# Optimization experiments

Hardware: AMD Instinct MI355X
Metric: run time of the kernel (lower is better)

## Reference

```python
import jax, jax.numpy as jnp
import numpy as np

D = 1024   # input_size == hidden_size (tied weights)
H = 1024
V = 32000
STEPS = 5  # mogrify_steps
B = 32
T = 64


def _mogrify(x, h, W, b):
    # W: [STEPS, H, H] (square since D == H), b: [STEPS, H]
    for i in range(STEPS):
        if (i + 1) % 2 == 0:
            h = 2.0 * jax.nn.sigmoid(x @ W[i].T + b[i]) * h
        else:
            x = 2.0 * jax.nn.sigmoid(h @ W[i].T + b[i]) * x
    return x, h


def _lstm_cell(x, h, c, W_ih, W_hh, b_ih, b_hh):
    g = x @ W_ih.T + b_ih + h @ W_hh.T + b_hh  # [B, 4H], gate order i,f,g,o
    i, f, gg, o = jnp.split(g, 4, axis=-1)
    c = jax.nn.sigmoid(f) * c + jax.nn.sigmoid(i) * jnp.tanh(gg)
    h = jax.nn.sigmoid(o) * jnp.tanh(c)
    return h, c


def setup_inputs() -> dict:
    key = jax.random.key(0)
    ks = jax.random.split(key, 16)
    s = 1.0 / np.sqrt(H)
    u = lambda k, shape: jax.random.uniform(k, shape, jnp.float32, -s, s)
    return {
        "seq": jax.random.randint(ks[0], (B, T), 0, V),
        "max_len": T,
        "emb": jax.random.normal(ks[1], (V, D), jnp.float32) * 0.02,  # tied with fc weight
        "mog1_W": u(ks[2], (STEPS, H, H)), "mog1_b": u(ks[3], (STEPS, H)),
        "W_ih1": u(ks[4], (4 * H, D)), "W_hh1": u(ks[5], (4 * H, H)),
        "b_ih1": u(ks[6], (4 * H,)), "b_hh1": u(ks[7], (4 * H,)),
        "mog2_W": u(ks[8], (STEPS, H, H)), "mog2_b": u(ks[9], (STEPS, H)),
        "W_ih2": u(ks[10], (4 * H, H)), "W_hh2": u(ks[11], (4 * H, H)),
        "b_ih2": u(ks[12], (4 * H,)), "b_hh2": u(ks[13], (4 * H,)),
        "fc_b": u(ks[14], (V,)),
    }


def reference(seq, max_len, emb, mog1_W, mog1_b, W_ih1, W_hh1, b_ih1, b_hh1,
              mog2_W, mog2_b, W_ih2, W_hh2, b_ih2, b_hh2, fc_b):
    batch = seq.shape[0]
    embed = emb[seq[:, :max_len]]              # [B, T, D]
    xs = jnp.transpose(embed, (1, 0, 2))       # [T, B, D]
    h1 = jnp.zeros((batch, H), embed.dtype)
    c1 = jnp.zeros((batch, H), embed.dtype)
    h2 = jnp.zeros((batch, H), embed.dtype)
    c2 = jnp.zeros((batch, H), embed.dtype)

    def step(carry, x):
        h1, c1, h2, c2 = carry
        x1, h1m = _mogrify(x, h1, mog1_W, mog1_b)
        h1, c1 = _lstm_cell(x1, h1m, c1, W_ih1, W_hh1, b_ih1, b_hh1)
        x2, h2m = _mogrify(h1, h2, mog2_W, mog2_b)
        h2, c2 = _lstm_cell(x2, h2m, c2, W_ih2, W_hh2, b_ih2, b_hh2)
        return (h1, c1, h2, c2), h2

    _, hs = jax.lax.scan(step, (h1, c1, h2, c2), xs)   # hs: [T, B, H]
    hidden_states = jnp.transpose(hs, (1, 0, 2))        # [B, T, H]
    # fc weight tied to embedding -> logits = h @ emb.T + b (single big GEMM)
    outputs = jnp.einsum('bth,vh->btv', hidden_states, emb) + fc_b  # [B, T, V]
    return outputs, hidden_states
```

## Files before the change

### kernel.cpp

```cpp
#include <hip/hip_runtime.h>

typedef short bf16x8 __attribute__((ext_vector_type(8)));
typedef float f32x4 __attribute__((ext_vector_type(4)));
typedef unsigned int u32;
typedef u32 u32x4 __attribute__((ext_vector_type(4)));
typedef unsigned short u16;
typedef unsigned long long u64;

static __device__ __forceinline__ unsigned short f2bf(float f) {
    unsigned int u = __float_as_uint(f);
    unsigned int r = (u + 0x7fffu + ((u >> 16) & 1u)) >> 16;
    return (unsigned short)r;
}
static __device__ __forceinline__ float sigmoidf_(float x) {
    return 1.0f / (1.0f + __expf(-x));
}
static __device__ __forceinline__ float tanhf_(float x) {
    return 2.0f / (1.0f + __expf(-2.0f * x)) - 1.0f;
}

static __device__ __forceinline__ u32 pkhi(float a, float b) {
    return (__float_as_uint(a) >> 16) | (__float_as_uint(b) & 0xffff0000u);
}
static __device__ __forceinline__ u32 pklo(float a, float b) {
    float la = a - __uint_as_float(__float_as_uint(a) & 0xffff0000u);
    float lb = b - __uint_as_float(__float_as_uint(b) & 0xffff0000u);
    return (__float_as_uint(la) >> 16) | (__float_as_uint(lb) & 0xffff0000u);
}
static __device__ __forceinline__ bf16x8 mkfrag(u32 a, u32 b, u32 c, u32 d) {
    u32x4 v = {a, b, c, d};
    return __builtin_bit_cast(bf16x8, v);
}

static __device__ __forceinline__ bf16x8 ldA(const u16* p) {
    u64 a = __hip_atomic_load((const u64*)p, __ATOMIC_RELAXED, __HIP_MEMORY_SCOPE_AGENT);
    u64 b = __hip_atomic_load((const u64*)(p + 4), __ATOMIC_RELAXED, __HIP_MEMORY_SCOPE_AGENT);
    union { u64 q[2]; bf16x8 v; } u;
    u.q[0] = a; u.q[1] = b;
    return u.v;
}
static __device__ __forceinline__ float ldc4(const float* p) {
    return __hip_atomic_load(p, __ATOMIC_RELAXED, __HIP_MEMORY_SCOPE_AGENT);
}
static __device__ __forceinline__ void stc4(float* p, float v) {
    __hip_atomic_store(p, v, __ATOMIC_RELAXED, __HIP_MEMORY_SCOPE_AGENT);
}
static __device__ __forceinline__ void stc2(u16* p, u16 v) {
    __hip_atomic_store(p, v, __ATOMIC_RELAXED, __HIP_MEMORY_SCOPE_AGENT);
}

static __device__ __forceinline__ void dma16(const float* g, float* l) {
    __builtin_amdgcn_global_load_lds((const __attribute__((address_space(1))) void*)g,
                                     (__attribute__((address_space(3))) void*)l, 16, 0, 0);
}

static __device__ __forceinline__ void arrD(u32* bar, int line) {
    asm volatile("s_waitcnt vmcnt(0) lgkmcnt(0)" ::: "memory");
    __builtin_amdgcn_s_barrier();
    if (threadIdx.x == 0)
        __hip_atomic_fetch_add(bar + line * 32, 1u, __ATOMIC_RELAXED, __HIP_MEMORY_SCOPE_AGENT);
}
static __device__ __forceinline__ void arrP(u32* bar, int line) {
    __builtin_amdgcn_s_barrier();
    if (threadIdx.x == 0)
        __hip_atomic_fetch_add(bar + line * 32, 1u, __ATOMIC_RELAXED, __HIP_MEMORY_SCOPE_AGENT);
}
static __device__ __forceinline__ void bwaitSD(u32* bar, int layer, bool glob, u32 target) {
    if (threadIdx.x < 64) {
        const bool on = glob || (threadIdx.x < 32);
        const int line = glob ? (int)threadIdx.x : layer * 32 + (int)(threadIdx.x & 31);
        const u32 tgt = glob ? (target << 8) : (target << 7);
        for (;;) {
            u32 v = on ? __hip_atomic_load(bar + line * 32, __ATOMIC_RELAXED,
                                           __HIP_MEMORY_SCOPE_AGENT) : 0u;
            v += __shfl_xor(v, 1);
            v += __shfl_xor(v, 2);
            v += __shfl_xor(v, 4);
            v += __shfl_xor(v, 8);
            v += __shfl_xor(v, 16);
            v += __shfl_xor(v, 32);
            if (v >= tgt) break;
            __builtin_amdgcn_s_sleep(1);
        }
    }
    __builtin_amdgcn_s_barrier();
    asm volatile("" ::: "memory");
}

static __device__ __forceinline__ void stage_mogF(const float* W, int jb, float* lbuf,
                                                  int lane, int wv) {
    int oct2 = lane >> 5, row = (lane >> 1) & 15, half = lane & 1;
#pragma unroll
    for (int i = 0; i < 16; ++i) {
        int og = wv * 16 + i;
        const float* src = W + (size_t)(jb + row) * 1024 + (og * 2 + oct2) * 8 + half * 4;
        dma16(src, lbuf + og * 256);
    }
}
static __device__ __forceinline__ void stage_l128(const float* Ws, int jb, int kb,
                                                  float* lbuf, int lane, int wv) {
    int half = lane & 1;
#pragma unroll
    for (int i = 0; i < 8; ++i) {
        int octl = wv * 4 + (i >> 1);
        int rh = i & 1;
        int rowc = rh * 32 + (lane >> 1);
        int grow = (rowc >> 4) * 1024 + jb + (rowc & 15);
        const float* src = Ws + (size_t)grow * 1024 + kb + octl * 8 + half * 4;
        dma16(src, lbuf + octl * 512 + rh * 256);
    }
}

static __device__ __forceinline__ void l_acts(const u16* aH, const u16* aL, int cidx,
                                              int lane, int wv, bf16x8 fr[4]) {
    const int col = lane & 15, kq4 = lane >> 4;
    size_t octa = (size_t)cidx * 16 + wv * 4 + kq4;
    const u16* pH = aH + (octa * 32 + col) * 8;
    const u16* pL = aL + (octa * 32 + col) * 8;
    fr[0] = ldA(pH);
    fr[1] = ldA(pH + 128);
    fr[2] = ldA(pL);
    fr[3] = ldA(pL + 128);
}
static __device__ __forceinline__ void l_mfma(const float* lbuf, const bf16x8 fr[4],
                                              int lane, int wv, f32x4 (&acc)[4][2]) {
    const int col = lane & 15, kq4 = lane >> 4;
    const float* wbase = lbuf + (wv * 4 + kq4) * 512;
#pragma unroll
    for (int rt = 0; rt < 4; ++rt) {
        const float* wp = wbase + (rt * 16 + col) * 8;
        f32x4 w0 = *(const f32x4*)wp, w1 = *(const f32x4*)(wp + 4);
        bf16x8 whi = mkfrag(pkhi(w0.x, w0.y), pkhi(w0.z, w0.w),
                            pkhi(w1.x, w1.y), pkhi(w1.z, w1.w));
        bf16x8 wlo = mkfrag(pklo(w0.x, w0.y), pklo(w0.z, w0.w),
                            pklo(w1.x, w1.y), pklo(w1.z, w1.w));
        acc[rt][0] = __builtin_amdgcn_mfma_f32_16x16x32_bf16(fr[0], whi, acc[rt][0], 0, 0, 0);
        acc[rt][0] = __builtin_amdgcn_mfma_f32_16x16x32_bf16(fr[2], whi, acc[rt][0], 0, 0, 0);
        acc[rt][0] = __builtin_amdgcn_mfma_f32_16x16x32_bf16(fr[0], wlo, acc[rt][0], 0, 0, 0);
        acc[rt][1] = __builtin_amdgcn_mfma_f32_16x16x32_bf16(fr[1], whi, acc[rt][1], 0, 0, 0);
        acc[rt][1] = __builtin_amdgcn_mfma_f32_16x16x32_bf16(fr[3], whi, acc[rt][1], 0, 0, 0);
        acc[rt][1] = __builtin_amdgcn_mfma_f32_16x16x32_bf16(fr[1], wlo, acc[rt][1], 0, 0, 0);
    }
}

struct RArgs {
    const float *m1W, *m1b, *Wih1, *Whh1, *bih1, *bhh1;
    const float *m2W, *m2b, *Wih2, *Whh2, *bih2, *bhh2;
    float* XTF;
    u16 *XTH, *XTL;
    float* stF;
    u16* stH;
    float* hs;
    u32* bar;
};

__global__ __launch_bounds__(256, 1) void reck(RArgs A) {
    __shared__ float wbuf[4][8192];
    __shared__ float red[4][32][16];

    const int tid = threadIdx.x, lane = tid & 63, wv = tid >> 6;
    const int col = lane & 15, kq4 = lane >> 4;
    const int blk = blockIdx.x;
    const int layer = blk >> 7;
    const int g = blk & 127;
    const bool isMog = g < 64;
    const int line = layer * 32 + (g & 31);
    const int jb = (g & 63) * 16;

    const float* mW  = layer ? A.m2W : A.m1W;
    const float* mb_ = layer ? A.m2b : A.m1b;
    const float* Wih = layer ? A.Wih2 : A.Wih1;
    const float* Whh = layer ? A.Whh2 : A.Whh1;
    const float* bih = layer ? A.bih2 : A.bih1;
    const float* bhh = layer ? A.bhh2 : A.bhh1;

    float* hF  = A.stF + layer * 32768;
    float* hmF = A.stF + 65536 + layer * 32768;
    float* cS  = A.stF + 131072 + layer * 32768;
    float* rFb = A.stF + 196608;
    u16* hH  = A.stH + layer * 32768;
    u16* hmH = A.stH + 65536 + layer * 32768;
    u16* rHb = A.stH + 131072;
    u16* hL  = A.stH + 196608 + layer * 32768;
    u16* hmL = A.stH + 262144 + layer * 32768;
    u16* rLb = A.stH + 327680;

    float* mbuf0 = &wbuf[0][0];
    float* mbuf1 = &wbuf[2][0];

    u32 bcnt = 0;
    int cur = 0;

    if (isMog) stage_mogF(mW, jb, mbuf0, lane, wv);

    for (int s = 0; s <= 64; ++s) {
        const bool act = layer ? (s > 0) : (s < 64);
        const int t = layer ? s - 1 : s;
        const int tt = act ? t : 0;
        const int rb = tt & 1;

        float* xF; u16 *xH, *xL;
        if (layer == 0) {
            xF = A.XTF + (size_t)tt * 32768;
            xH = A.XTH + (size_t)tt * 32768;
            xL = A.XTL + (size_t)tt * 32768;
        } else {
            xF = rFb + rb * 32768;
            xH = rHb + rb * 32768;
            xL = rLb + rb * 32768;
        }

        if (isMog) {
            for (int ph = 0; ph < 5; ++ph) {
                float* wsrc = cur ? mbuf1 : mbuf0;
                float* wdst = cur ? mbuf0 : mbuf1;
                if (act) {
                    const u16 *gH, *gL; const float* srcF; float* dF; u16 *dH, *dL;
                    switch (ph) {
                        case 0:  gH = hH;  gL = hL;  srcF = xF;  dF = xF;  dH = xH;  dL = xL;  break;
                        case 1:  gH = xH;  gL = xL;  srcF = hF;  dF = hmF; dH = hmH; dL = hmL; break;
                        case 2:  gH = hmH; gL = hmL; srcF = xF;  dF = xF;  dH = xH;  dL = xL;  break;
                        case 3:  gH = xH;  gL = xL;  srcF = hmF; dF = hmF; dH = hmH; dL = hmL; break;
                        default: gH = hmH; gL = hmL; srcF = xF;  dF = xF;  dH = xH;  dL = xL;  break;
                    }
                    bf16x8 AH0[8], AH1[8], AL0[8], AL1[8];
#pragma unroll
                    for (int kt = 0; kt < 8; ++kt) {
                        int octc = wv * 32 + kt * 4 + kq4;
                        const u16* pH = gH + ((size_t)octc * 32 + col) * 8;
                        const u16* pL = gL + ((size_t)octc * 32 + col) * 8;
                        AH0[kt] = ldA(pH);  AH1[kt] = ldA(pH + 128);
                        AL0[kt] = ldA(pL);  AL1[kt] = ldA(pL + 128);
                    }
                    asm volatile("s_waitcnt vmcnt(63)" ::: "memory");
                    f32x4 a0 = {0.f, 0.f, 0.f, 0.f}, a1 = {0.f, 0.f, 0.f, 0.f};
#pragma unroll
                    for (int kt = 0; kt < 8; ++kt) {
                        int octc = wv * 32 + kt * 4 + kq4;
                        const float* wp = wsrc + octc * 128 + col * 8;
                        f32x4 w0 = *(const f32x4*)wp, w1 = *(const f32x4*)(wp + 4);
                        bf16x8 whi = mkfrag(pkhi(w0.x, w0.y), pkhi(w0.z, w0.w),
                                            pkhi(w1.x, w1.y), pkhi(w1.z, w1.w));
                        bf16x8 wlo = mkfrag(pklo(w0.x, w0.y), pklo(w0.z, w0.w),
                                            pklo(w1.x, w1.y), pklo(w1.z, w1.w));
                        a0 = __builtin_amdgcn_mfma_f32_16x16x32_bf16(AH0[kt], whi, a0, 0, 0, 0);
                        a0 = __builtin_amdgcn_mfma_f32_16x16x32_bf16(AL0[kt], whi, a0, 0, 0, 0);
                        a0 = __builtin_amdgcn_mfma_f32_16x16x32_bf16(AH0[kt], wlo, a0, 0, 0, 0);
                        a1 = __builtin_amdgcn_mfma_f32_16x16x32_bf16(AH1[kt], whi, a1, 0, 0, 0);
                        a1 = __builtin_amdgcn_mfma_f32_16x16x32_bf16(AL1[kt], whi, a1, 0, 0, 0);
                        a1 = __builtin_amdgcn_mfma_f32_16x16x32_bf16(AH1[kt], wlo, a1, 0, 0, 0);
                    }
#pragma unroll
                    for (int mh = 0; mh < 2; ++mh) {
                        f32x4 av = mh ? a1 : a0;
#pragma unroll
                        for (int r = 0; r < 4; ++r)
                            red[wv][mh * 16 + kq4 * 4 + r][col] = av[r];
                    }
                    __syncthreads();
#pragma unroll
                    for (int uu = 0; uu < 2; ++uu) {
                        int u = tid + uu * 256;
                        int jj = u & 15, bb = u >> 4;
                        float sv = red[0][bb][jj] + red[1][bb][jj]
                                 + red[2][bb][jj] + red[3][bb][jj];
                        int d = jb + jj;
                        sv += mb_[ph * 1024 + d];
                        float gate = 2.0f * sigmoidf_(sv);
                        size_t pidx = ((size_t)(d >> 3) * 32 + bb) * 8 + (d & 7);
                        float val = gate * ldc4(srcF + pidx);
                        stc4(dF + pidx, val);
                        u32 uv = __float_as_uint(val);
                        stc2(dH + pidx, (u16)(uv >> 16));
                        float lov = val - __uint_as_float(uv & 0xffff0000u);
                        stc2(dL + pidx, (u16)(__float_as_uint(lov) >> 16));
                    }
                    arrD(A.bar, line);
                } else {
                    arrP(A.bar, line);
                }
                ++bcnt;
                stage_mogF(mW + (size_t)((ph + 1) % 5) * 1048576, jb, wdst, lane, wv);
                bwaitSD(A.bar, layer, false, bcnt);
                cur ^= 1;
            }
            arrP(A.bar, line);
            ++bcnt;
            bwaitSD(A.bar, layer, true, bcnt);
        } else {
            const bool firstAct = act && (layer ? (s == 1) : (s == 0));
            const bool nextAct = layer ? (s < 64) : (s < 63);
            if (firstAct) {
#pragma unroll
                for (int c = 0; c < 3; ++c)
                    stage_l128(Whh, jb, c * 128, &wbuf[c][0], lane, wv);
            }
#pragma unroll
            for (int p = 0; p < 4; ++p) {
                arrP(A.bar, line);
                ++bcnt;
                bwaitSD(A.bar, layer, false, bcnt);
            }
            arrP(A.bar, line);
            ++bcnt;
            u32 g5t = bcnt;
            f32x4 acc[4][2];
#pragma unroll
            for (int rt = 0; rt < 4; ++rt) {
                acc[rt][0] = (f32x4){0.f, 0.f, 0.f, 0.f};
                acc[rt][1] = (f32x4){0.f, 0.f, 0.f, 0.f};
            }
            bf16x8 frA[4], frB[4];
            if (act) {
                l_acts(hmH, hmL, 0, lane, wv, frA);
#pragma unroll
                for (int c = 0; c < 8; ++c) {
                    if (c < 7) {
                        if (c & 1) l_acts(hmH, hmL, c + 1, lane, wv, frA);
                        else       l_acts(hmH, hmL, c + 1, lane, wv, frB);
                    }
                    asm volatile("s_waitcnt vmcnt(32)" ::: "memory");
                    int cn = c + 3;
                    if (cn < 8) stage_l128(Whh, jb, cn * 128, &wbuf[cn & 3][0], lane, wv);
                    else        stage_l128(Wih, jb, (cn - 8) * 128, &wbuf[cn & 3][0], lane, wv);
                    if (c & 1) l_mfma(&wbuf[c & 3][0], frB, lane, wv, acc);
                    else       l_mfma(&wbuf[c & 3][0], frA, lane, wv, acc);
                }
            }
            bwaitSD(A.bar, layer, false, g5t);
            if (act) {
                l_acts(xH, xL, 0, lane, wv, frA);
#pragma unroll
                for (int c = 0; c < 8; ++c) {
                    if (c < 7) {
                        if (c & 1) l_acts(xH, xL, c + 1, lane, wv, frA);
                        else       l_acts(xH, xL, c + 1, lane, wv, frB);
                    }
                    asm volatile("s_waitcnt vmcnt(32)" ::: "memory");
                    int cn = c + 3;
                    if (cn < 8) stage_l128(Wih, jb, cn * 128, &wbuf[cn & 3][0], lane, wv);
                    if (c & 1) l_mfma(&wbuf[c & 3][0], frB, lane, wv, acc);
                    else       l_mfma(&wbuf[c & 3][0], frA, lane, wv, acc);
                }
                float gv[2][4];
#pragma unroll
                for (int gt = 0; gt < 4; ++gt) {
                    __syncthreads();
#pragma unroll
                    for (int mh = 0; mh < 2; ++mh) {
                        f32x4 av = acc[gt][mh];
#pragma unroll
                        for (int r = 0; r < 4; ++r)
                            red[wv][mh * 16 + kq4 * 4 + r][col] = av[r];
                    }
                    __syncthreads();
#pragma unroll
                    for (int uu = 0; uu < 2; ++uu) {
                        int u = tid + uu * 256;
                        gv[uu][gt] = red[0][u >> 4][u & 15] + red[1][u >> 4][u & 15]
                                   + red[2][u >> 4][u & 15] + red[3][u >> 4][u & 15];
                    }
                }
#pragma unroll
                for (int uu = 0; uu < 2; ++uu) {
                    int u = tid + uu * 256;
                    int cell = u & 15, bb = u >> 4;
                    int d = jb + cell;
                    float gi = gv[uu][0] + bih[d] + bhh[d];
                    float gf = gv[uu][1] + bih[1024 + d] + bhh[1024 + d];
                    float gg = gv[uu][2] + bih[2048 + d] + bhh[2048 + d];
                    float go = gv[uu][3] + bih[3072 + d] + bhh[3072 + d];
                    int cidx = d * 32 + bb;
                    float cn = sigmoidf_(gf) * cS[cidx] + sigmoidf_(gi) * tanhf_(gg);
                    cS[cidx] = cn;
                    float hn = sigmoidf_(go) * tanhf_(cn);
                    size_t pidx = ((size_t)(d >> 3) * 32 + bb) * 8 + (d & 7);
                    u32 uv = __float_as_uint(hn);
                    u16 hhi = (u16)(uv >> 16);
                    float lov = hn - __uint_as_float(uv & 0xffff0000u);
                    u16 hlo = (u16)(__float_as_uint(lov) >> 16);
                    stc4(hF + pidx, hn);
                    stc2(hH + pidx, hhi);
                    stc2(hL + pidx, hlo);
                    if (layer == 0) {
                        int wb = s & 1;
                        stc4(rFb + wb * 32768 + pidx, hn);
                        stc2(rHb + wb * 32768 + pidx, hhi);
                        stc2(rLb + wb * 32768 + pidx, hlo);
                    } else {
                        A.hs[(size_t)bb * 65536 + (size_t)t * 1024 + d] = hn;
                    }
                }
                arrD(A.bar, line);
                ++bcnt;
                if (nextAct) {
#pragma unroll
                    for (int c = 0; c < 3; ++c)
                        stage_l128(Whh, jb, c * 128, &wbuf[c][0], lane, wv);
                }
            } else {
                arrP(A.bar, line);
                ++bcnt;
            }
            bwaitSD(A.bar, layer, true, bcnt);
        }
    }
}

__global__ __launch_bounds__(256) void gather_embed(const int* __restrict__ seq,
                                                    const float* __restrict__ emb,
                                                    float* __restrict__ XTF,
                                                    u16* __restrict__ XTH,
                                                    u16* __restrict__ XTL) {
    int t = blockIdx.x;
#pragma unroll 4
    for (int i = 0; i < 16; ++i) {
        int u = i * 256 + threadIdx.x;
        int oct = u >> 5, b = u & 31;
        int row = seq[b * 64 + t];
        const float* sp = emb + (size_t)row * 1024 + oct * 8;
        float4 f0 = *(const float4*)sp;
        float4 f1 = *(const float4*)(sp + 4);
        size_t base = (size_t)t * 32768 + ((size_t)oct * 32 + b) * 8;
        *(float4*)(XTF + base) = f0;
        *(float4*)(XTF + base + 4) = f1;
        u32x4 hi = {pkhi(f0.x, f0.y), pkhi(f0.z, f0.w), pkhi(f1.x, f1.y), pkhi(f1.z, f1.w)};
        u32x4 lo = {pklo(f0.x, f0.y), pklo(f0.z, f0.w), pklo(f1.x, f1.y), pklo(f1.z, f1.w)};
        *(u32x4*)(XTH + base) = hi;
        *(u32x4*)(XTL + base) = lo;
    }
}

__global__ __launch_bounds__(256) void f32_to_bf16(const float* __restrict__ in,
                                                   unsigned short* __restrict__ out, int n) {
    int i = (blockIdx.x * 256 + threadIdx.x) * 8;
    if (i + 7 < n) {
        float4 f0 = *(const float4*)(in + i);
        float4 f1 = *(const float4*)(in + i + 4);
        bf16x8 v;
        v[0] = (short)f2bf(f0.x); v[1] = (short)f2bf(f0.y);
        v[2] = (short)f2bf(f0.z); v[3] = (short)f2bf(f0.w);
        v[4] = (short)f2bf(f1.x); v[5] = (short)f2bf(f1.y);
        v[6] = (short)f2bf(f1.z); v[7] = (short)f2bf(f1.w);
        *(bf16x8*)(out + i) = v;
    }
}

__global__ __launch_bounds__(256) void out_proj(const unsigned short* __restrict__ hsb,
                                                const float* __restrict__ emb,
                                                const float* __restrict__ fcb,
                                                float* __restrict__ out) {
    __shared__ unsigned short Al[128 * 40];
    __shared__ unsigned short Bl[128 * 40];
    int tid = threadIdx.x;
    int n0 = blockIdx.x * 128;
    int m0 = blockIdx.y * 128;
    int wid = tid >> 6, l = tid & 63;
    int wm = wid >> 1, wn = wid & 1;
    int c16 = l & 15, kg = l >> 4;

    f32x4 acc[4][4];
#pragma unroll
    for (int i = 0; i < 4; i++)
#pragma unroll
        for (int j = 0; j < 4; j++) acc[i][j] = (f32x4){0.f, 0.f, 0.f, 0.f};

    for (int k0 = 0; k0 < 1024; k0 += 32) {
#pragma unroll
        for (int i = 0; i < 2; i++) {
            int id = i * 256 + tid;
            int r = id >> 2, ccc = id & 3;
            *(bf16x8*)&Al[r * 40 + ccc * 8] =
                *(const bf16x8*)(hsb + (size_t)(m0 + r) * 1024 + k0 + ccc * 8);
        }
#pragma unroll
        for (int i = 0; i < 2; i++) {
            int id = i * 256 + tid;
            int r = id >> 2, ccc = id & 3;
            const float* src = emb + (size_t)(n0 + r) * 1024 + k0 + ccc * 8;
            float4 f0 = *(const float4*)(src);
            float4 f1 = *(const float4*)(src + 4);
            bf16x8 v;
            v[0] = (short)f2bf(f0.x); v[1] = (short)f2bf(f0.y);
            v[2] = (short)f2bf(f0.z); v[3] = (short)f2bf(f0.w);
            v[4] = (short)f2bf(f1.x); v[5] = (short)f2bf(f1.y);
            v[6] = (short)f2bf(f1.z); v[7] = (short)f2bf(f1.w);
            *(bf16x8*)&Bl[r * 40 + ccc * 8] = v;
        }
        __syncthreads();

        bf16x8 afr[4], bfr[4];
#pragma unroll
        for (int i = 0; i < 4; i++)
            afr[i] = *(const bf16x8*)&Al[(wm * 64 + i * 16 + c16) * 40 + kg * 8];
#pragma unroll
        for (int j = 0; j < 4; j++)
            bfr[j] = *(const bf16x8*)&Bl[(wn * 64 + j * 16 + c16) * 40 + kg * 8];
#pragma unroll
        for (int i = 0; i < 4; i++)
#pragma unroll
            for (int j = 0; j < 4; j++)
                acc[i][j] = __builtin_amdgcn_mfma_f32_16x16x32_bf16(afr[i], bfr[j], acc[i][j], 0, 0, 0);
        __syncthreads();
    }

#pragma unroll
    for (int i = 0; i < 4; i++) {
        int row = m0 + wm * 64 + i * 16 + kg * 4;
#pragma unroll
        for (int j = 0; j < 4; j++) {
            int col = n0 + wn * 64 + j * 16 + c16;
            float fb = fcb[col];
#pragma unroll
            for (int r = 0; r < 4; r++)
                out[(size_t)(row + r) * 32000 + col] = acc[i][j][r] + fb;
        }
    }
}

extern "C" void kernel_launch(void* const* d_in, const int* in_sizes, int n_in,
                              void* d_out, int out_size, void* d_ws, size_t ws_size,
                              hipStream_t stream) {
    const int*   seq    = (const int*)d_in[0];
    const float* emb    = (const float*)d_in[2];
    const float* mog1_W = (const float*)d_in[3];
    const float* mog1_b = (const float*)d_in[4];
    const float* W_ih1  = (const float*)d_in[5];
    const float* W_hh1  = (const float*)d_in[6];
    const float* b_ih1  = (const float*)d_in[7];
    const float* b_hh1  = (const float*)d_in[8];
    const float* mog2_W = (const float*)d_in[9];
    const float* mog2_b = (const float*)d_in[10];
    const float* W_ih2  = (const float*)d_in[11];
    const float* W_hh2  = (const float*)d_in[12];
    const float* b_ih2  = (const float*)d_in[13];
    const float* b_hh2  = (const float*)d_in[14];
    const float* fc_b   = (const float*)d_in[15];

    char* ws = (char*)d_ws;
    float* XTF = (float*)ws;
    u16*   XTH = (u16*)(ws + 8388608);
    u16*   XTL = (u16*)(ws + 12582912);
    float* stF = (float*)(ws + 16777216);
    u16*   stH = (u16*)(ws + 17825792);
    u32*   bar = (u32*)(ws + 18874368);
    unsigned short* hsb = (unsigned short*)(ws + 18890752);

    float* out0 = (float*)d_out;
    float* hs   = out0 + 65536000LL;

    (void)hipMemsetAsync(stF, 0, 1835008, stream);
    (void)hipMemsetAsync(bar, 0, 16384, stream);

    gather_embed<<<64, 256, 0, stream>>>(seq, emb, XTF, XTH, XTL);

    RArgs a;
    a.m1W = mog1_W; a.m1b = mog1_b;
    a.Wih1 = W_ih1; a.Whh1 = W_hh1; a.bih1 = b_ih1; a.bhh1 = b_hh1;
    a.m2W = mog2_W; a.m2b = mog2_b;
    a.Wih2 = W_ih2; a.Whh2 = W_hh2; a.bih2 = b_ih2; a.bhh2 = b_hh2;
    a.XTF = XTF; a.XTH = XTH; a.XTL = XTL;
    a.stF = stF; a.stH = stH; a.hs = hs; a.bar = bar;

    reck<<<256, 256, 0, stream>>>(a);

    f32_to_bf16<<<1024, 256, 0, stream>>>(hs, hsb, 2097152);
    out_proj<<<dim3(250, 16), 256, 0, stream>>>(hsb, emb, fc_b, out0);
}
```

Baseline: 4.222 ms.

## Replace all-block barrier polling with master-based generation counters in recurrent kernel

Swaps the grid barrier, where every block polls and sums all arrival lines, for a scheme in which one master block per group sums the arrival counters and publishes a generation value that other blocks poll with a single load. LSTM-gate blocks no longer take part in the per-phase mogrifier barriers and only wait on the mogrifier generation counter right before they consume its outputs. The prefetch of the next mogrifier weight slice and the source-value loads are moved ahead of the MFMA loop so they overlap compute. This is meant to cut polling traffic and barrier latency on the serial critical path, at the cost of an extra hop through the master and more workspace space for barrier counters.

```diff
diff --git a/kernel.cpp b/kernel.cpp
--- a/kernel.cpp
+++ b/kernel.cpp
@@ -54,33 +54,39 @@
                                      (__attribute__((address_space(3))) void*)l, 16, 0, 0);
 }
 
-static __device__ __forceinline__ void arrD(u32* bar, int line) {
-    asm volatile("s_waitcnt vmcnt(0) lgkmcnt(0)" ::: "memory");
-    __builtin_amdgcn_s_barrier();
-    if (threadIdx.x == 0)
-        __hip_atomic_fetch_add(bar + line * 32, 1u, __ATOMIC_RELAXED, __HIP_MEMORY_SCOPE_AGENT);
-}
-static __device__ __forceinline__ void arrP(u32* bar, int line) {
-    __builtin_amdgcn_s_barrier();
-    if (threadIdx.x == 0)
-        __hip_atomic_fetch_add(bar + line * 32, 1u, __ATOMIC_RELAXED, __HIP_MEMORY_SCOPE_AGENT);
-}
-static __device__ __forceinline__ void bwaitSD(u32* bar, int layer, bool glob, u32 target) {
-    if (threadIdx.x < 64) {
-        const bool on = glob || (threadIdx.x < 32);
-        const int line = glob ? (int)threadIdx.x : layer * 32 + (int)(threadIdx.x & 31);
-        const u32 tgt = glob ? (target << 8) : (target << 7);
-        for (;;) {
-            u32 v = on ? __hip_atomic_load(bar + line * 32, __ATOMIC_RELAXED,
-                                           __HIP_MEMORY_SCOPE_AGENT) : 0u;
-            v += __shfl_xor(v, 1);
-            v += __shfl_xor(v, 2);
-            v += __shfl_xor(v, 4);
-            v += __shfl_xor(v, 8);
-            v += __shfl_xor(v, 16);
-            v += __shfl_xor(v, 32);
-            if (v >= tgt) break;
-            __builtin_amdgcn_s_sleep(1);
+static __device__ __forceinline__ void lineAdd(u32* bar, int idx, u32 v) {
+    __hip_atomic_fetch_add(bar + idx, v, __ATOMIC_RELAXED, __HIP_MEMORY_SCOPE_AGENT);
+}
+static __device__ __forceinline__ u32 lsum(u32* bar, int baseIdx, int nl) {
+    u32 v = 0;
+    if ((int)threadIdx.x < nl)
+        v = __hip_atomic_load(bar + baseIdx + (int)threadIdx.x * 32,
+                              __ATOMIC_RELAXED, __HIP_MEMORY_SCOPE_AGENT);
+    v += __shfl_xor(v, 1);
+    v += __shfl_xor(v, 2);
+    v += __shfl_xor(v, 4);
+    v += __shfl_xor(v, 8);
+    v += __shfl_xor(v, 16);
+    v += __shfl_xor(v, 32);
+    return v;
+}
+static __device__ __forceinline__ void waitGen(u32* bar, int lineBase, int nl, int genIdx,
+                                               bool master, u32 t, u32 need) {
+    if (master) {
+        if (threadIdx.x < 64) {
+            for (;;) {
+                u32 v = lsum(bar, lineBase, nl);
+                if (v >= need) break;
+                __builtin_amdgcn_s_sleep(1);
+            }
+            if (threadIdx.x == 0)
+                __hip_atomic_store(bar + genIdx, t, __ATOMIC_RELAXED, __HIP_MEMORY_SCOPE_AGENT);
+        }
+    } else {
+        if (threadIdx.x == 0) {
+            while (__hip_atomic_load(bar + genIdx, __ATOMIC_RELAXED,
+                                     __HIP_MEMORY_SCOPE_AGENT) < t)
+                __builtin_amdgcn_s_sleep(1);
         }
     }
     __builtin_amdgcn_s_barrier();
@@ -164,7 +170,12 @@
     const int layer = blk >> 7;
     const int g = blk & 127;
     const bool isMog = g < 64;
-    const int line = layer * 32 + (g & 31);
+    const bool masterM = (g == 0);
+    const bool masterG = (g == 64);
+    const int moglineIdx = layer * 1024 + (g & 31) * 32;
+    const int g6lineIdx  = 2048 + (blk & 63) * 32;
+    const int genMi = 4096 + layer * 32;
+    const int genGi = 4224 + layer * 32;
     const int jb = (g & 63) * 16;
 
     const float* mW  = layer ? A.m2W : A.m1W;
@@ -188,10 +199,14 @@
     float* mbuf0 = &wbuf[0][0];
     float* mbuf1 = &wbuf[2][0];
 
-    u32 bcnt = 0;
+    u32 mgbase = 0;
     int cur = 0;
 
-    if (isMog) stage_mogF(mW, jb, mbuf0, lane, wv);
+    if (isMog) {
+        stage_mogF(mW, jb, mbuf0, lane, wv);
+        asm volatile("s_waitcnt vmcnt(0)" ::: "memory");
+    }
+    __builtin_amdgcn_s_barrier();
 
     for (int s = 0; s <= 64; ++s) {
         const bool act = layer ? (s > 0) : (s < 64);
@@ -211,10 +226,10 @@
         }
 
         if (isMog) {
-            for (int ph = 0; ph < 5; ++ph) {
-                float* wsrc = cur ? mbuf1 : mbuf0;
-                float* wdst = cur ? mbuf0 : mbuf1;
-                if (act) {
+            if (act) {
+                for (int ph = 0; ph < 5; ++ph) {
+                    float* wsrc = cur ? mbuf1 : mbuf0;
+                    float* wdst = cur ? mbuf0 : mbuf1;
                     const u16 *gH, *gL; const float* srcF; float* dF; u16 *dH, *dL;
                     switch (ph) {
                         case 0:  gH = hH;  gL = hL;  srcF = xF;  dF = xF;  dH = xH;  dL = xL;  break;
@@ -232,7 +247,17 @@
                         AH0[kt] = ldA(pH);  AH1[kt] = ldA(pH + 128);
                         AL0[kt] = ldA(pL);  AL1[kt] = ldA(pL + 128);
                     }
-                    asm volatile("s_waitcnt vmcnt(63)" ::: "memory");
+                    float sF[2];
+                    size_t pidxv[2];
+#pragma unroll
+                    for (int uu = 0; uu < 2; ++uu) {
+                        int u = tid + uu * 256;
+                        int jj = u & 15, bb = u >> 4;
+                        int d = jb + jj;
+                        pidxv[uu] = ((size_t)(d >> 3) * 32 + bb) * 8 + (d & 7);
+                        sF[uu] = ldc4(srcF + pidxv[uu]);
+                    }
+                    stage_mogF(mW + (size_t)((ph + 1) % 5) * 1048576, jb, wdst, lane, wv);
                     f32x4 a0 = {0.f, 0.f, 0.f, 0.f}, a1 = {0.f, 0.f, 0.f, 0.f};
 #pragma unroll
                     for (int kt = 0; kt < 8; ++kt) {
@@ -267,51 +292,60 @@
                         int d = jb + jj;
                         sv += mb_[ph * 1024 + d];
                         float gate = 2.0f * sigmoidf_(sv);
-                        size_t pidx = ((size_t)(d >> 3) * 32 + bb) * 8 + (d & 7);
-                        float val = gate * ldc4(srcF + pidx);
-                        stc4(dF + pidx, val);
+                        float val = gate * sF[uu];
+                        stc4(dF + pidxv[uu], val);
                         u32 uv = __float_as_uint(val);
-                        stc2(dH + pidx, (u16)(uv >> 16));
+                        stc2(dH + pidxv[uu], (u16)(uv >> 16));
                         float lov = val - __uint_as_float(uv & 0xffff0000u);
-                        stc2(dL + pidx, (u16)(__float_as_uint(lov) >> 16));
-                    }
-                    arrD(A.bar, line);
-                } else {
-                    arrP(A.bar, line);
-                }
-                ++bcnt;
-                stage_mogF(mW + (size_t)((ph + 1) % 5) * 1048576, jb, wdst, lane, wv);
-                bwaitSD(A.bar, layer, false, bcnt);
-                cur ^= 1;
+                        stc2(dL + pidxv[uu], (u16)(__float_as_uint(lov) >> 16));
+                    }
+                    asm volatile("s_waitcnt vmcnt(0) lgkmcnt(0)" ::: "memory");
+                    __builtin_amdgcn_s_barrier();
+                    if (tid == 0) lineAdd(A.bar, moglineIdx, 1);
+                    if (ph < 4)
+                        waitGen(A.bar, layer * 1024, 32, genMi, masterM,
+                                mgbase + ph + 1, (mgbase + ph + 1) << 6);
+                    cur ^= 1;
+                }
+                if (masterM) {
+                    if (tid < 64) {
+                        for (;;) {
+                            u32 v = lsum(A.bar, layer * 1024, 32);
+                            if (v >= ((mgbase + 5) << 6)) break;
+                            __builtin_amdgcn_s_sleep(1);
+                        }
+                        if (tid == 0)
+                            __hip_atomic_store(A.bar + genMi, mgbase + 5,
+                                               __ATOMIC_RELAXED, __HIP_MEMORY_SCOPE_AGENT);
+                    }
+                }
+                __builtin_amdgcn_s_barrier();
+                if (tid == 0) lineAdd(A.bar, g6lineIdx, 1);
+            } else {
+                __builtin_amdgcn_s_barrier();
+                if (tid == 0) {
+                    lineAdd(A.bar, moglineIdx, 5);
+                    lineAdd(A.bar, g6lineIdx, 1);
+                }
             }
-            arrP(A.bar, line);
-            ++bcnt;
-            bwaitSD(A.bar, layer, true, bcnt);
+            waitGen(A.bar, 2048, 64, genGi, false, (u32)(s + 1), (u32)(s + 1) << 8);
         } else {
-            const bool firstAct = act && (layer ? (s == 1) : (s == 0));
-            const bool nextAct = layer ? (s < 64) : (s < 63);
-            if (firstAct) {
-#pragma unroll
-                for (int c = 0; c < 3; ++c)
-                    stage_l128(Whh, jb, c * 128, &wbuf[c][0], lane, wv);
-            }
-#pragma unroll
-            for (int p = 0; p < 4; ++p) {
-                arrP(A.bar, line);
-                ++bcnt;
-                bwaitSD(A.bar, layer, false, bcnt);
-            }
-            arrP(A.bar, line);
-            ++bcnt;
-            u32 g5t = bcnt;
-            f32x4 acc[4][2];
-#pragma unroll
-            for (int rt = 0; rt < 4; ++rt) {
-                acc[rt][0] = (f32x4){0.f, 0.f, 0.f, 0.f};
-                acc[rt][1] = (f32x4){0.f, 0.f, 0.f, 0.f};
-            }
-            bf16x8 frA[4], frB[4];
             if (act) {
+                const bool firstAct = layer ? (s == 1) : (s == 0);
+                const bool nextAct = layer ? (s < 64) : (s < 63);
+                if (firstAct) {
+#pragma unroll
+                    for (int c = 0; c < 3; ++c)
+                        stage_l128(Whh, jb, c * 128, &wbuf[c][0], lane, wv);
+                }
+                waitGen(A.bar, layer * 1024, 32, genMi, false, mgbase + 4, 0);
+                f32x4 acc[4][2];
+#pragma unroll
+                for (int rt = 0; rt < 4; ++rt) {
+                    acc[rt][0] = (f32x4){0.f, 0.f, 0.f, 0.f};
+                    acc[rt][1] = (f32x4){0.f, 0.f, 0.f, 0.f};
+                }
+                bf16x8 frA[4], frB[4];
                 l_acts(hmH, hmL, 0, lane, wv, frA);
 #pragma unroll
                 for (int c = 0; c < 8; ++c) {
@@ -326,9 +360,7 @@
                     if (c & 1) l_mfma(&wbuf[c & 3][0], frB, lane, wv, acc);
                     else       l_mfma(&wbuf[c & 3][0], frA, lane, wv, acc);
                 }
-            }
-            bwaitSD(A.bar, layer, false, g5t);
-            if (act) {
+                waitGen(A.bar, layer * 1024, 32, genMi, false, mgbase + 5, 0);
                 l_acts(xH, xL, 0, lane, wv, frA);
 #pragma unroll
                 for (int c = 0; c < 8; ++c) {
@@ -391,19 +423,21 @@
                         A.hs[(size_t)bb * 65536 + (size_t)t * 1024 + d] = hn;
                     }
                 }
-                arrD(A.bar, line);
-                ++bcnt;
+                asm volatile("s_waitcnt vmcnt(0) lgkmcnt(0)" ::: "memory");
+                __builtin_amdgcn_s_barrier();
+                if (tid == 0) lineAdd(A.bar, g6lineIdx, 1);
                 if (nextAct) {
 #pragma unroll
                     for (int c = 0; c < 3; ++c)
                         stage_l128(Whh, jb, c * 128, &wbuf[c][0], lane, wv);
                 }
             } else {
-                arrP(A.bar, line);
-                ++bcnt;
+                __builtin_amdgcn_s_barrier();
+                if (tid == 0) lineAdd(A.bar, g6lineIdx, 1);
             }
-            bwaitSD(A.bar, layer, true, bcnt);
+            waitGen(A.bar, 2048, 64, genGi, masterG, (u32)(s + 1), (u32)(s + 1) << 8);
         }
+        mgbase += 5;
     }
 }
 
@@ -544,13 +578,13 @@
     float* stF = (float*)(ws + 16777216);
     u16*   stH = (u16*)(ws + 17825792);
     u32*   bar = (u32*)(ws + 18874368);
-    unsigned short* hsb = (unsigned short*)(ws + 18890752);
+    unsigned short* hsb = (unsigned short*)(ws + 18907136);
 
     float* out0 = (float*)d_out;
     float* hs   = out0 + 65536000LL;
 
     (void)hipMemsetAsync(stF, 0, 1835008, stream);
-    (void)hipMemsetAsync(bar, 0, 16384, stream);
+    (void)hipMemsetAsync(bar, 0, 32768, stream);
 
     gather_embed<<<64, 256, 0, stream>>>(seq, emb, XTF, XTH, XTL);
 
```

Result: slower. 4.434 ms (+5.0%).
